# Optimization experiments

Measured on AMD Instinct MI355X. Metric: run time of the kernel, lower is better.

The kernel has to match this reference:

```python
import jax, jax.numpy as jnp
import numpy as np

OMEGA_ENC = 0.01   # Encoder.omega
OMEGA_K = 0.1      # KernelMLP.omega
N0, E0 = 4096, 16384     # level-0 graph
N1, E1 = 1024, 8192      # level-1 (pooled) graph
F_IN, H, LAT, DIM = 8, 64, 32, 3
F = H + DIM              # conv input features (x || pos)


def _glorot(key, shape):
    s = jnp.sqrt(2.0 / (shape[0] + shape[-1]))
    return (jax.random.normal(key, shape) * s).astype(jnp.float32)


def setup_inputs() -> dict:
    key = jax.random.key(0)
    ks = jax.random.split(key, 24)
    inp = {
        "x": jax.random.normal(ks[0], (N0, F_IN), jnp.float32),
        "pos": jax.random.normal(ks[1], (N0, DIM), jnp.float32),
        "edge_index": jax.random.randint(ks[2], (2, E0), 0, N0),
        "pool_edge_index1": jax.random.randint(ks[3], (2, E1), 0, N1),
        "pool_pos1": jax.random.normal(ks[4], (N1, DIM), jnp.float32),
        "pool_keep_idx0": jnp.sort(jax.random.randint(ks[5], (N1,), 0, N0)),
        "lin0_w": _glorot(ks[6], (F_IN, H)),
        "lin0_b": 0.01 * jax.random.normal(ks[7], (H,), jnp.float32),
        "lin1_w": _glorot(ks[8], (H, LAT)),
        "lin1_b": 0.01 * jax.random.normal(ks[9], (LAT,), jnp.float32),
    }
    k = 10
    for i in range(2):
        inp[f"conv{i}_k_w0"] = _glorot(ks[k], (DIM + 1, H))
        inp[f"conv{i}_k_b0"] = 0.01 * jax.random.normal(ks[k + 1], (H,), jnp.float32)
        inp[f"conv{i}_k_w1"] = _glorot(ks[k + 2], (H, H))
        inp[f"conv{i}_k_b1"] = 0.01 * jax.random.normal(ks[k + 3], (H,), jnp.float32)
        inp[f"conv{i}_k_w2"] = _glorot(ks[k + 4], (H, F))
        inp[f"conv{i}_k_b2"] = 0.01 * jax.random.normal(ks[k + 5], (F,), jnp.float32)
        inp[f"conv{i}_bias"] = jnp.zeros((H,), jnp.float32)  # zeros() init in torch
        k += 6
    return inp


def _with_self_loops(ei, n):
    # add_remaining_self_loops: input edges are assumed self-loop-free
    loops = jnp.arange(n, dtype=ei.dtype)
    return jnp.concatenate([ei, jnp.stack([loops, loops])], axis=1)


def _kernel_conv(xf, ei, pos, n, w0, b0, w1, b1, w2, b2, bias):
    src, dst = ei[0], ei[1]
    rel = pos[dst] - pos[src]                               # [E,3]
    zero = jnp.all(rel == 0.0, axis=1)                      # self loops -> rho=0, nan phi in torch
    rel_s = jnp.where(zero[:, None], 1.0, rel)              # safe values (avoid nan grads)
    rho = jnp.sqrt(jnp.sum(rel_s * rel_s, axis=1))
    theta = jnp.arctan2(rel_s[:, 1], rel_s[:, 0])
    phi = jnp.arcsin(jnp.clip(rel_s[:, 2] / rho, -1.0, 1.0))
    # torch sets theta/phi to 0 where phi is nan (rho==0); rho itself is 0 there
    rho = jnp.where(zero, 0.0, rho)
    theta = jnp.where(zero, 0.0, theta)
    phi = jnp.where(zero, 0.0, phi)
    feats = jnp.stack([rho, theta / jnp.pi, phi / jnp.pi], axis=1)   # [E,3]
    # KernelMLP lin0 on (feats || channel_id), evaluated for all out channels at once
    base = feats @ w0[:DIM] + b0                            # [E,H]
    ch = jnp.arange(H, dtype=xf.dtype)                      # out_channels == H
    h0 = jnp.sin(OMEGA_K * (base[None] + ch[:, None, None] * w0[DIM][None, None]))  # [C,E,H]
    h1 = jnp.sin(OMEGA_K * (jnp.einsum('ceh,hk->cek', h0, w1) + b1))                # [C,E,H]
    x_j = xf[src]                                           # [E,F]
    # msg[e,c] = (lin2(h1[c,e]) * x_j[e]).sum(); lin2 folded into the contraction
    msg = jnp.einsum('ceh,hf,ef->ec', h1, w2, x_j) + (x_j @ b2)[:, None]            # [E,C]
    return jax.ops.segment_sum(msg, dst, num_segments=n) + bias


def reference(x, edge_index, pos, pool_edge_index1, pool_pos1, pool_keep_idx0,
              lin0_w, lin0_b, lin1_w, lin1_b,
              conv0_k_w0, conv0_k_b0, conv0_k_w1, conv0_k_b1, conv0_k_w2, conv0_k_b2, conv0_bias,
              conv1_k_w0, conv1_k_b0, conv1_k_w1, conv1_k_b1, conv1_k_w2, conv1_k_b2, conv1_bias):
    n0 = x.shape[0]
    h = jnp.sin(OMEGA_ENC * (x @ lin0_w + lin0_b))
    ei0 = _with_self_loops(edge_index, n0)
    h = jnp.sin(OMEGA_ENC * _kernel_conv(jnp.concatenate([h, pos], 1), ei0, pos, n0,
                                         conv0_k_w0, conv0_k_b0, conv0_k_w1, conv0_k_b1,
                                         conv0_k_w2, conv0_k_b2, conv0_bias))
    # max_pool_neighbor_x: per-node max over neighbors incl. self (self loops in ei0)
    h = jax.ops.segment_max(h[ei0[0]], ei0[1], num_segments=n0)[pool_keep_idx0]
    n1 = pool_pos1.shape[0]
    ei1 = _with_self_loops(pool_edge_index1, n1)
    h = jnp.sin(OMEGA_ENC * _kernel_conv(jnp.concatenate([h, pool_pos1], 1), ei1, pool_pos1, n1,
                                         conv1_k_w0, conv1_k_b0, conv1_k_w1, conv1_k_b1,
                                         conv1_k_w2, conv1_k_b2, conv1_bias))
    return jnp.sin(OMEGA_ENC * (h @ lin1_w + lin1_b))   # [N1, LAT]
```

## Files before the change

### kernel.cpp

```cpp
#include <hip/hip_runtime.h>
#include <hip/hip_fp16.h>

#define N0C 4096
#define E0C 16384
#define N1C 1024
#define E1C 8192
#define HC 64
#define FINC 8
#define LATC 32
#define FC 67
#define E0T (E0C + N0C)
#define E1T (E1C + N1C)

typedef float f32x4 __attribute__((ext_vector_type(4)));
typedef _Float16 f16x8 __attribute__((ext_vector_type(8)));

__global__ __launch_bounds__(256) void k_prep(
    const float* __restrict__ x, const float* __restrict__ l0w,
    const float* __restrict__ l0b, const float* __restrict__ posp,
    const float* __restrict__ c0w2, const float* __restrict__ c0b2,
    const float* __restrict__ c0w0, const float* __restrict__ c1w0,
    const float* __restrict__ c0w1, const float* __restrict__ c1w1,
    _Float16* __restrict__ bC0, _Float16* __restrict__ bS0,
    _Float16* __restrict__ bC1, _Float16* __restrict__ bS1,
    _Float16* __restrict__ w1f0, _Float16* __restrict__ w1f1,
    float* __restrict__ tN, float* __restrict__ dN,
    float* __restrict__ accz) {
  if (blockIdx.x < 256) {
    __shared__ float w2s[64][69];
    __shared__ float xr[4][64];
    const int tid = threadIdx.x;
    const int wave = __builtin_amdgcn_readfirstlane(tid >> 6), lane = tid & 63;
    for (int idx = tid; idx < HC * FC; idx += 256)
      w2s[idx / FC][idx % FC] = c0w2[idx];
    __syncthreads();
#pragma unroll
    for (int i = 0; i < 4; ++i) {
      const int n = (blockIdx.x * 4 + wave) + i * 1024;
      float a = l0b[lane];
#pragma unroll
      for (int f = 0; f < FINC; ++f) a = fmaf(x[n * FINC + f], l0w[f * HC + lane], a);
      xr[wave][lane] = sinf(0.01f * a);
      __builtin_amdgcn_wave_barrier();
      const float px = posp[n * 3], py = posp[n * 3 + 1], pz = posp[n * 3 + 2];
      float tl = 0.f, ds = 0.f;
#pragma unroll 8
      for (int f = 0; f < HC; ++f) {
        float xv = xr[wave][f];
        tl = fmaf(xv, w2s[lane][f], tl);
        ds = fmaf(xv, c0b2[f], ds);
      }
      tl = fmaf(px, w2s[lane][64], fmaf(py, w2s[lane][65], fmaf(pz, w2s[lane][66], tl)));
      ds = fmaf(px, c0b2[64], fmaf(py, c0b2[65], fmaf(pz, c0b2[66], ds)));
      tN[n * HC + lane] = tl;
      if (lane == 0) dN[n] = ds;
      __builtin_amdgcn_wave_barrier();
    }
  } else if (blockIdx.x < 320) {
    int id = (blockIdx.x - 256) * 256 + threadIdx.x;
    if (id < 8192) {
      int lvl = id >> 12, r = id & 4095;
      int fi = r >> 9, lane = (r >> 3) & 63, j = r & 7;
      int nt = fi & 3, ks = fi >> 2;
      int c = nt * 16 + (lane & 15);
      int h = ks * 32 + (lane >> 4) * 8 + j;
      const float* w = lvl ? c1w0 : c0w0;
      float s, cv;
      sincosf(0.1f * (float)c * w[3 * HC + h], &s, &cv);
      (lvl ? bC1 : bC0)[r] = (_Float16)cv;
      (lvl ? bS1 : bS0)[r] = (_Float16)s;
    } else {
      int r0 = id - 8192;
      int lvl = r0 >> 12, r = r0 & 4095;
      int fi = r >> 9, lane = (r >> 3) & 63, j = r & 7;
      int ms = fi & 3, ks = fi >> 2;
      int h = ks * 32 + (lane >> 4) * 8 + j;
      int kout = ms * 16 + (lane & 15);
      const float* w = lvl ? c1w1 : c0w1;
      (lvl ? w1f1 : w1f0)[r] = (_Float16)(0.1f * w[h * HC + kout]);
    }
  } else {
    int t = (blockIdx.x - 320) * 256 + threadIdx.x;
    f32x4 z = {0.f, 0.f, 0.f, 0.f};
    f32x4* zp = (f32x4*)accz;
    zp[t] = z;
    zp[t + 49152] = z;
    zp[t + 98304] = z;
  }
}

__global__ __launch_bounds__(256, 3) void k_conv(
    const int* __restrict__ ei, int E, int eTot,
    const float* __restrict__ posp,
    const float* __restrict__ tN, const float* __restrict__ dN,
    const float* __restrict__ kw0, const float* __restrict__ kb0,
    const _Float16* __restrict__ bC, const _Float16* __restrict__ bS,
    const _Float16* __restrict__ w1f, const float* __restrict__ b1,
    float* __restrict__ acc_out) {
  __shared__ __attribute__((aligned(16))) _Float16 bCs[4096], bSs[4096];
  __shared__ __attribute__((aligned(16))) _Float16 scS[4][2][64], scC[4][2][64];
  const int tid = threadIdx.x;
  const int wave = __builtin_amdgcn_readfirstlane(tid >> 6), lane = tid & 63;
  const int q = lane >> 4;
  for (int idx = tid; idx < 512; idx += 256) {
    ((f16x8*)bCs)[idx] = ((const f16x8*)bC)[idx];
    ((f16x8*)bSs)[idx] = ((const f16x8*)bS)[idx];
  }
  f16x8 w1r[8];
#pragma unroll
  for (int f = 0; f < 8; ++f) w1r[f] = *(const f16x8*)(w1f + ((f << 6) + lane) * 8);
  f32x4 bbq[4];
#pragma unroll
  for (int ms = 0; ms < 4; ++ms) {
    f32x4 t = *(const f32x4*)(b1 + ms * 16 + q * 4);
    bbq[ms] = t * 0.1f;
  }
  const float kb0v = kb0[lane];
  const float kw0x = kw0[lane], kw0y = kw0[HC + lane], kw0z = kw0[2 * HC + lane];
  __syncthreads();

  const int nW = gridDim.x * 4;
  int e = blockIdx.x * 4 + wave;
  if (e >= eTot) return;

  auto stg = [&](int ee, int& sN, int& dTo, float& sv, float& cv, float& dv) {
    int s, d2;
    if (ee < E) { s = ei[ee]; d2 = ei[E + ee]; } else { s = ee - E; d2 = s; }
    sN = s;
    dTo = d2;
    const float px = posp[s * 3], py = posp[s * 3 + 1], pz = posp[s * 3 + 2];
    const float rx = posp[d2 * 3] - px;
    const float ry = posp[d2 * 3 + 1] - py;
    const float rz = posp[d2 * 3 + 2] - pz;
    float f0 = 0.f, f1 = 0.f, f2 = 0.f;
    if (!(rx == 0.f && ry == 0.f && rz == 0.f)) {
      const float INV_PI = 0.3183098861837907f;
      const float PI_F = 3.14159265358979f;
      const float PI_2 = 1.5707963267948966f;
      float rho = sqrtf(rx * rx + ry * ry + rz * rz);
      float ax = fabsf(rx), ay = fabsf(ry);
      float mx = fmaxf(ax, ay), mn = fminf(ax, ay);
      float zr = mn * __builtin_amdgcn_rcpf(mx);
      float z2 = zr * zr;
      float pa = fmaf(z2, -0.0040540580f, 0.0218612288f);
      pa = fmaf(z2, pa, -0.0559098861f);
      pa = fmaf(z2, pa, 0.0964200441f);
      pa = fmaf(z2, pa, -0.1390853351f);
      pa = fmaf(z2, pa, 0.1994653599f);
      pa = fmaf(z2, pa, -0.3332985605f);
      pa = fmaf(z2, pa, 0.9999993329f);
      float at = pa * zr;
      at = (ay > ax) ? (PI_2 - at) : at;
      at = (rx < 0.f) ? (PI_F - at) : at;
      float th = copysignf(at, ry);
      float zz = rz * __builtin_amdgcn_rcpf(rho);
      float az = fminf(fabsf(zz), 1.0f);
      float sq = sqrtf(1.0f - az);
      float pp = fmaf(az, -0.0187293f, 0.0742610f);
      pp = fmaf(az, pp, -0.2121144f);
      pp = fmaf(az, pp, 1.5707288f);
      float as = PI_2 - sq * pp;
      float ph = copysignf(as, zz);
      f0 = rho; f1 = th * INV_PI; f2 = ph * INV_PI;
    }
    float base = fmaf(f0, kw0x, fmaf(f1, kw0y, fmaf(f2, kw0z, kb0v)));
    __sincosf(0.1f * base, &sv, &cv);
    dv = dN[s];
  };

  int s0, d0;
  float sv0, cv0, dv0;
  stg(e, s0, d0, sv0, cv0, dv0);
  int buf = 0;
  scS[wave][0][lane] = (_Float16)sv0;
  scC[wave][0][lane] = (_Float16)cv0;
  __builtin_amdgcn_wave_barrier();

  while (true) {
    const int en = e + nW;
    const bool more = en < eTot;
    f32x4 tr[4];
    {
      const float* trp = tN + (size_t)s0 * HC;
#pragma unroll
      for (int ms = 0; ms < 4; ++ms) tr[ms] = *(const f32x4*)(trp + ms * 16 + q * 4);
    }
    int s1 = 0, d1 = 0;
    float sv1 = 0.f, cv1 = 0.f, dv1 = 0.f;
    if (more) {
      stg(en, s1, d1, sv1, cv1, dv1);
      scS[wave][buf ^ 1][lane] = (_Float16)sv1;
      scC[wave][buf ^ 1][lane] = (_Float16)cv1;
    }
    __builtin_amdgcn_wave_barrier();

    f32x4 acc[4][4];
#pragma unroll
    for (int ms = 0; ms < 4; ++ms)
#pragma unroll
      for (int nt = 0; nt < 4; ++nt) acc[ms][nt] = bbq[ms];
#pragma unroll
    for (int ks = 0; ks < 2; ++ks) {
      f16x8 sv8 = *(const f16x8*)&scS[wave][buf][ks * 32 + q * 8];
      f16x8 cv8 = *(const f16x8*)&scC[wave][buf][ks * 32 + q * 8];
      f16x8 bf[4];
#pragma unroll
      for (int nt = 0; nt < 4; ++nt) {
        f16x8 cb = *(const f16x8*)&bCs[((ks * 4 + nt) * 64 + lane) * 8];
        f16x8 sb = *(const f16x8*)&bSs[((ks * 4 + nt) * 64 + lane) * 8];
        bf[nt] = sv8 * cb + cv8 * sb;
      }
#pragma unroll
      for (int ms = 0; ms < 4; ++ms)
#pragma unroll
        for (int nt = 0; nt < 4; ++nt)
          acc[ms][nt] = __builtin_amdgcn_mfma_f32_16x16x32_f16(
              w1r[ks * 4 + ms], bf[nt], acc[ms][nt], 0, 0, 0);
    }

    float snt0 = 0.f, snt1 = 0.f, snt2 = 0.f, snt3 = 0.f;
#pragma unroll
    for (int ms = 0; ms < 4; ++ms) {
#pragma unroll
      for (int r = 0; r < 4; ++r) {
        float tt = tr[ms][r];
        snt0 = fmaf(__sinf(acc[ms][0][r]), tt, snt0);
        snt1 = fmaf(__sinf(acc[ms][1][r]), tt, snt1);
        snt2 = fmaf(__sinf(acc[ms][2][r]), tt, snt2);
        snt3 = fmaf(__sinf(acc[ms][3][r]), tt, snt3);
      }
    }
    snt0 += __shfl_xor(snt0, 16, 64); snt0 += __shfl_xor(snt0, 32, 64);
    snt1 += __shfl_xor(snt1, 16, 64); snt1 += __shfl_xor(snt1, 32, 64);
    snt2 += __shfl_xor(snt2, 16, 64); snt2 += __shfl_xor(snt2, 32, 64);
    snt3 += __shfl_xor(snt3, 16, 64); snt3 += __shfl_xor(snt3, 32, 64);
    float val = (q == 0) ? snt0 : (q == 1) ? snt1 : (q == 2) ? snt2 : snt3;
    atomicAdd(acc_out + (size_t)d0 * HC + lane, val + dv0);

    if (!more) break;
    e = en; s0 = s1; d0 = d1; dv0 = dv1; buf ^= 1;
  }
}

__global__ __launch_bounds__(256) void k_pool(
    const int* __restrict__ ei, const float* __restrict__ acc0,
    const float* __restrict__ bias, unsigned int* __restrict__ pooled) {
  const int wave = threadIdx.x >> 6, lane = threadIdx.x & 63;
  const float bz = bias[lane];
  for (int e = blockIdx.x * 4 + wave; e < E0T; e += gridDim.x * 4) {
    int s, d;
    if (e < E0C) { s = ei[e]; d = ei[E0C + e]; } else { s = e - E0C; d = s; }
    float v = sinf(0.01f * (acc0[(size_t)s * HC + lane] + bz));
    unsigned int b = __float_as_uint(v);
    unsigned int key = (b & 0x80000000u) ? ~b : (b | 0x80000000u);
    atomicMax(pooled + (size_t)d * HC + lane, key);
  }
}

__global__ __launch_bounds__(256) void k_t1(
    const unsigned int* __restrict__ pooled, const int* __restrict__ keep,
    const float* __restrict__ ppos, const float* __restrict__ c1w2,
    const float* __restrict__ c1b2, float* __restrict__ tN, float* __restrict__ dN) {
  __shared__ float w2s[64][69];
  __shared__ float xr[4][64];
  const int tid = threadIdx.x;
  const int wave = __builtin_amdgcn_readfirstlane(tid >> 6), lane = tid & 63;
  for (int idx = tid; idx < HC * FC; idx += 256)
    w2s[idx / FC][idx % FC] = c1w2[idx];
  const int i = blockIdx.x * 4 + wave;
  const int n = keep[i];
  unsigned int key = pooled[(size_t)n * HC + lane];
  unsigned int b = (key & 0x80000000u) ? (key & 0x7FFFFFFFu) : ~key;
  xr[wave][lane] = __uint_as_float(b);
  __syncthreads();
  const float px = ppos[i * 3], py = ppos[i * 3 + 1], pz = ppos[i * 3 + 2];
  float tl = 0.f, ds = 0.f;
#pragma unroll 8
  for (int f = 0; f < HC; ++f) {
    float xv = xr[wave][f];
    tl = fmaf(xv, w2s[lane][f], tl);
    ds = fmaf(xv, c1b2[f], ds);
  }
  tl = fmaf(px, w2s[lane][64], fmaf(py, w2s[lane][65], fmaf(pz, w2s[lane][66], tl)));
  ds = fmaf(px, c1b2[64], fmaf(py, c1b2[65], fmaf(pz, c1b2[66], ds)));
  tN[i * HC + lane] = tl;
  if (lane == 0) dN[i] = ds;
}

__global__ __launch_bounds__(256) void k_final(
    const float* __restrict__ acc1, const float* __restrict__ bias,
    const float* __restrict__ l1w, const float* __restrict__ l1b,
    float* __restrict__ outp) {
  __shared__ float hr[4][64];
  const int wave = threadIdx.x >> 6, lane = threadIdx.x & 63;
  const int node = blockIdx.x * 4 + wave;
  hr[wave][lane] = sinf(0.01f * (acc1[(size_t)node * HC + lane] + bias[lane]));
  __syncthreads();
  if (lane < LATC) {
    const float* h = hr[wave];
    float o = l1b[lane];
#pragma unroll 8
    for (int c = 0; c < HC; ++c) o = fmaf(h[c], l1w[c * LATC + lane], o);
    outp[node * LATC + lane] = sinf(0.01f * o);
  }
}

extern "C" void kernel_launch(void* const* d_in, const int* in_sizes, int n_in,
                              void* d_out, int out_size, void* d_ws, size_t ws_size,
                              hipStream_t stream) {
  (void)in_sizes; (void)n_in; (void)out_size; (void)ws_size;
  const float* x    = (const float*)d_in[0];
  const float* pos  = (const float*)d_in[1];
  const int*   ei   = (const int*)d_in[2];
  const int*   pei  = (const int*)d_in[3];
  const float* ppos = (const float*)d_in[4];
  const int*   keep = (const int*)d_in[5];
  const float* l0w  = (const float*)d_in[6];
  const float* l0b  = (const float*)d_in[7];
  const float* l1w  = (const float*)d_in[8];
  const float* l1b  = (const float*)d_in[9];
  const float* c0w0 = (const float*)d_in[10];
  const float* c0b0 = (const float*)d_in[11];
  const float* c0w1 = (const float*)d_in[12];
  const float* c0b1 = (const float*)d_in[13];
  const float* c0w2 = (const float*)d_in[14];
  const float* c0b2 = (const float*)d_in[15];
  const float* c0bias = (const float*)d_in[16];
  const float* c1w0 = (const float*)d_in[17];
  const float* c1b0 = (const float*)d_in[18];
  const float* c1w1 = (const float*)d_in[19];
  const float* c1b1 = (const float*)d_in[20];
  const float* c1w2 = (const float*)d_in[21];
  const float* c1b2 = (const float*)d_in[22];
  const float* c1bias = (const float*)d_in[23];
  float* outp = (float*)d_out;

  char* p = (char*)d_ws;
  auto carve = [&](size_t bytes) -> char* {
    char* r = p;
    p += (bytes + 255) & ~(size_t)255;
    return r;
  };
  float* tN0  = (float*)carve((size_t)N0C * HC * 4);
  float* dN0  = (float*)carve((size_t)N0C * 4);
  float* tN1  = (float*)carve((size_t)N1C * HC * 4);
  float* dN1  = (float*)carve((size_t)N1C * 4);
  _Float16* bC0  = (_Float16*)carve(4096 * 2);
  _Float16* bS0  = (_Float16*)carve(4096 * 2);
  _Float16* bC1  = (_Float16*)carve(4096 * 2);
  _Float16* bS1  = (_Float16*)carve(4096 * 2);
  _Float16* w1f0 = (_Float16*)carve(4096 * 2);
  _Float16* w1f1 = (_Float16*)carve(4096 * 2);
  float* acc0 = (float*)carve((size_t)N0C * HC * 4);
  unsigned int* pooled = (unsigned int*)carve((size_t)N0C * HC * 4);
  float* acc1 = (float*)carve((size_t)N1C * HC * 4);

  k_prep<<<512, 256, 0, stream>>>(x, l0w, l0b, pos, c0w2, c0b2,
                                  c0w0, c1w0, c0w1, c1w1,
                                  bC0, bS0, bC1, bS1, w1f0, w1f1,
                                  tN0, dN0, acc0);
  k_conv<<<1536, 256, 0, stream>>>(ei, E0C, E0T, pos, tN0, dN0, c0w0, c0b0,
                                   bC0, bS0, w1f0, c0b1, acc0);
  k_pool<<<1280, 256, 0, stream>>>(ei, acc0, c0bias, pooled);
  k_t1<<<N1C / 4, 256, 0, stream>>>(pooled, keep, ppos, c1w2, c1b2, tN1, dN1);
  k_conv<<<768, 256, 0, stream>>>(pei, E1C, E1T, ppos, tN1, dN1, c1w0, c1b0,
                                  bC1, bS1, w1f1, c1b1, acc1);
  k_final<<<N1C / 4, 256, 0, stream>>>(acc1, c1bias, l1w, l1b, outp);
}
```

Baseline: 163.2 us.

## Fuse level-1 node transform into conv kernel and shrink level-0 conv grid

Removes the separate k_t1 launch by computing each edge's level-1 node transform (pooled features times w2 plus position terms, and the bias dot product) inside the templated conv kernel, staged through shared memory. This saves one launch and the tN1/dN1 round trip through global memory. In exchange, the 64x67 matvec is recomputed per edge instead of per node, with 9216 edges against 1024 nodes. The extra shared memory for the w2 copy may also lower occupancy. The level-0 conv grid is also halved from 1536 to 768 blocks.

```diff
diff --git a/kernel.cpp b/kernel.cpp
--- a/kernel.cpp
+++ b/kernel.cpp
@@ -89,16 +89,22 @@
   }
 }
 
+template <bool L1>
 __global__ __launch_bounds__(256, 3) void k_conv(
     const int* __restrict__ ei, int E, int eTot,
     const float* __restrict__ posp,
     const float* __restrict__ tN, const float* __restrict__ dN,
+    const unsigned* __restrict__ pooled, const int* __restrict__ keep,
+    const float* __restrict__ w2, const float* __restrict__ b2,
     const float* __restrict__ kw0, const float* __restrict__ kb0,
     const _Float16* __restrict__ bC, const _Float16* __restrict__ bS,
     const _Float16* __restrict__ w1f, const float* __restrict__ b1,
     float* __restrict__ acc_out) {
   __shared__ __attribute__((aligned(16))) _Float16 bCs[4096], bSs[4096];
   __shared__ __attribute__((aligned(16))) _Float16 scS[4][2][64], scC[4][2][64];
+  __shared__ float w2s[64][69];
+  __shared__ float xrs[4][2][64];
+  __shared__ float trow[4][64];
   const int tid = threadIdx.x;
   const int wave = __builtin_amdgcn_readfirstlane(tid >> 6), lane = tid & 63;
   const int q = lane >> 4;
@@ -106,6 +112,10 @@
     ((f16x8*)bCs)[idx] = ((const f16x8*)bC)[idx];
     ((f16x8*)bSs)[idx] = ((const f16x8*)bS)[idx];
   }
+  if constexpr (L1) {
+    for (int idx = tid; idx < HC * FC; idx += 256)
+      w2s[idx / FC][idx % FC] = w2[idx];
+  }
   f16x8 w1r[8];
 #pragma unroll
   for (int f = 0; f < 8; ++f) w1r[f] = *(const f16x8*)(w1f + ((f << 6) + lane) * 8);
@@ -117,13 +127,19 @@
   }
   const float kb0v = kb0[lane];
   const float kw0x = kw0[lane], kw0y = kw0[HC + lane], kw0z = kw0[2 * HC + lane];
+  float b2v = 0.f, b2x = 0.f, b2y = 0.f, b2z = 0.f;
+  if constexpr (L1) {
+    b2v = b2[lane];
+    b2x = b2[64]; b2y = b2[65]; b2z = b2[66];
+  }
   __syncthreads();
 
   const int nW = gridDim.x * 4;
   int e = blockIdx.x * 4 + wave;
   if (e >= eTot) return;
 
-  auto stg = [&](int ee, int& sN, int& dTo, float& sv, float& cv, float& dv) {
+  auto stg = [&](int ee, int bufIdx, int& sN, int& dTo, float& sv, float& cv,
+                 float& dv, float& opx, float& opy, float& opz) {
     int s, d2;
     if (ee < E) { s = ei[ee]; d2 = ei[E + ee]; } else { s = ee - E; d2 = s; }
     sN = s;
@@ -132,6 +148,7 @@
     const float rx = posp[d2 * 3] - px;
     const float ry = posp[d2 * 3 + 1] - py;
     const float rz = posp[d2 * 3 + 2] - pz;
+    opx = px; opy = py; opz = pz;
     float f0 = 0.f, f1 = 0.f, f2 = 0.f;
     if (!(rx == 0.f && ry == 0.f && rz == 0.f)) {
       const float INV_PI = 0.3183098861837907f;
@@ -165,12 +182,25 @@
     }
     float base = fmaf(f0, kw0x, fmaf(f1, kw0y, fmaf(f2, kw0z, kb0v)));
     __sincosf(0.1f * base, &sv, &cv);
-    dv = dN[s];
+    if constexpr (L1) {
+      int kn = keep[s];
+      unsigned key = pooled[(size_t)kn * HC + lane];
+      unsigned bb = (key & 0x80000000u) ? (key & 0x7FFFFFFFu) : ~key;
+      float xv = __uint_as_float(bb);
+      xrs[wave][bufIdx][lane] = xv;
+      float dp = xv * b2v;
+      dp += __shfl_xor(dp, 1, 64);  dp += __shfl_xor(dp, 2, 64);
+      dp += __shfl_xor(dp, 4, 64);  dp += __shfl_xor(dp, 8, 64);
+      dp += __shfl_xor(dp, 16, 64); dp += __shfl_xor(dp, 32, 64);
+      dv = dp + fmaf(px, b2x, fmaf(py, b2y, pz * b2z));
+    } else {
+      dv = dN[s];
+    }
   };
 
   int s0, d0;
-  float sv0, cv0, dv0;
-  stg(e, s0, d0, sv0, cv0, dv0);
+  float sv0, cv0, dv0, p0x, p0y, p0z;
+  stg(e, 0, s0, d0, sv0, cv0, dv0, p0x, p0y, p0z);
   int buf = 0;
   scS[wave][0][lane] = (_Float16)sv0;
   scC[wave][0][lane] = (_Float16)cv0;
@@ -179,20 +209,33 @@
   while (true) {
     const int en = e + nW;
     const bool more = en < eTot;
-    f32x4 tr[4];
-    {
-      const float* trp = tN + (size_t)s0 * HC;
-#pragma unroll
-      for (int ms = 0; ms < 4; ++ms) tr[ms] = *(const f32x4*)(trp + ms * 16 + q * 4);
-    }
     int s1 = 0, d1 = 0;
-    float sv1 = 0.f, cv1 = 0.f, dv1 = 0.f;
+    float sv1 = 0.f, cv1 = 0.f, dv1 = 0.f, p1x = 0.f, p1y = 0.f, p1z = 0.f;
     if (more) {
-      stg(en, s1, d1, sv1, cv1, dv1);
+      stg(en, buf ^ 1, s1, d1, sv1, cv1, dv1, p1x, p1y, p1z);
       scS[wave][buf ^ 1][lane] = (_Float16)sv1;
       scC[wave][buf ^ 1][lane] = (_Float16)cv1;
     }
     __builtin_amdgcn_wave_barrier();
+
+    f32x4 tr[4];
+    if constexpr (L1) {
+      float tl = 0.f;
+#pragma unroll 8
+      for (int f = 0; f < HC; ++f) tl = fmaf(xrs[wave][buf][f], w2s[lane][f], tl);
+      tl = fmaf(p0x, w2s[lane][64],
+           fmaf(p0y, w2s[lane][65], fmaf(p0z, w2s[lane][66], tl)));
+      trow[wave][lane] = tl;
+      __builtin_amdgcn_wave_barrier();
+#pragma unroll
+      for (int ms = 0; ms < 4; ++ms)
+        tr[ms] = *(const f32x4*)&trow[wave][ms * 16 + q * 4];
+      __builtin_amdgcn_wave_barrier();
+    } else {
+      const float* trp = tN + (size_t)s0 * HC;
+#pragma unroll
+      for (int ms = 0; ms < 4; ++ms) tr[ms] = *(const f32x4*)(trp + ms * 16 + q * 4);
+    }
 
     f32x4 acc[4][4];
 #pragma unroll
@@ -238,7 +281,9 @@
     atomicAdd(acc_out + (size_t)d0 * HC + lane, val + dv0);
 
     if (!more) break;
-    e = en; s0 = s1; d0 = d1; dv0 = dv1; buf ^= 1;
+    e = en; s0 = s1; d0 = d1; dv0 = dv1;
+    p0x = p1x; p0y = p1y; p0z = p1z;
+    buf ^= 1;
   }
 }
 
@@ -255,36 +300,6 @@
     unsigned int key = (b & 0x80000000u) ? ~b : (b | 0x80000000u);
     atomicMax(pooled + (size_t)d * HC + lane, key);
   }
-}
-
-__global__ __launch_bounds__(256) void k_t1(
-    const unsigned int* __restrict__ pooled, const int* __restrict__ keep,
-    const float* __restrict__ ppos, const float* __restrict__ c1w2,
-    const float* __restrict__ c1b2, float* __restrict__ tN, float* __restrict__ dN) {
-  __shared__ float w2s[64][69];
-  __shared__ float xr[4][64];
-  const int tid = threadIdx.x;
-  const int wave = __builtin_amdgcn_readfirstlane(tid >> 6), lane = tid & 63;
-  for (int idx = tid; idx < HC * FC; idx += 256)
-    w2s[idx / FC][idx % FC] = c1w2[idx];
-  const int i = blockIdx.x * 4 + wave;
-  const int n = keep[i];
-  unsigned int key = pooled[(size_t)n * HC + lane];
-  unsigned int b = (key & 0x80000000u) ? (key & 0x7FFFFFFFu) : ~key;
-  xr[wave][lane] = __uint_as_float(b);
-  __syncthreads();
-  const float px = ppos[i * 3], py = ppos[i * 3 + 1], pz = ppos[i * 3 + 2];
-  float tl = 0.f, ds = 0.f;
-#pragma unroll 8
-  for (int f = 0; f < HC; ++f) {
-    float xv = xr[wave][f];
-    tl = fmaf(xv, w2s[lane][f], tl);
-    ds = fmaf(xv, c1b2[f], ds);
-  }
-  tl = fmaf(px, w2s[lane][64], fmaf(py, w2s[lane][65], fmaf(pz, w2s[lane][66], tl)));
-  ds = fmaf(px, c1b2[64], fmaf(py, c1b2[65], fmaf(pz, c1b2[66], ds)));
-  tN[i * HC + lane] = tl;
-  if (lane == 0) dN[i] = ds;
 }
 
 __global__ __launch_bounds__(256) void k_final(
@@ -343,8 +358,6 @@
   };
   float* tN0  = (float*)carve((size_t)N0C * HC * 4);
   float* dN0  = (float*)carve((size_t)N0C * 4);
-  float* tN1  = (float*)carve((size_t)N1C * HC * 4);
-  float* dN1  = (float*)carve((size_t)N1C * 4);
   _Float16* bC0  = (_Float16*)carve(4096 * 2);
   _Float16* bS0  = (_Float16*)carve(4096 * 2);
   _Float16* bC1  = (_Float16*)carve(4096 * 2);
@@ -359,11 +372,12 @@
                                   c0w0, c1w0, c0w1, c1w1,
                                   bC0, bS0, bC1, bS1, w1f0, w1f1,
                                   tN0, dN0, acc0);
-  k_conv<<<1536, 256, 0, stream>>>(ei, E0C, E0T, pos, tN0, dN0, c0w0, c0b0,
-                                   bC0, bS0, w1f0, c0b1, acc0);
+  k_conv<false><<<768, 256, 0, stream>>>(ei, E0C, E0T, pos, tN0, dN0,
+                                         nullptr, nullptr, nullptr, nullptr,
+                                         c0w0, c0b0, bC0, bS0, w1f0, c0b1, acc0);
   k_pool<<<1280, 256, 0, stream>>>(ei, acc0, c0bias, pooled);
-  k_t1<<<N1C / 4, 256, 0, stream>>>(pooled, keep, ppos, c1w2, c1b2, tN1, dN1);
-  k_conv<<<768, 256, 0, stream>>>(pei, E1C, E1T, ppos, tN1, dN1, c1w0, c1b0,
-                                  bC1, bS1, w1f1, c1b1, acc1);
+  k_conv<true><<<768, 256, 0, stream>>>(pei, E1C, E1T, ppos, nullptr, nullptr,
+                                        pooled, keep, c1w2, c1b2,
+                                        c1w0, c1b0, bC1, bS1, w1f1, c1b1, acc1);
   k_final<<<N1C / 4, 256, 0, stream>>>(acc1, c1bias, l1w, l1b, outp);
 }
```

Measured after the change: 163.7 us, median of 2. About the same (+0.3%).
